# Kernel optimization log

Measured on AMD Instinct MI355X. Metric: run time of the kernel, lower is better.

The kernel has to match this reference:

```python
import jax, jax.numpy as jnp
import numpy as np

D_MODEL = 1024
NUM_HEADS = 16
D_K = D_MODEL // NUM_HEADS
D_FF = 4096
EPS = 1e-5


def _layer_norm(x, g, b):
    mu = jnp.mean(x, axis=-1, keepdims=True)
    var = jnp.mean(jnp.square(x - mu), axis=-1, keepdims=True)
    return (x - mu) * jax.lax.rsqrt(var + EPS) * g + b


def setup_inputs() -> dict:
    key = jax.random.key(0)
    ks = jax.random.split(key, 16)
    s = 0.02
    inp = {
        "x": jax.random.normal(ks[0], (2, 2048, D_MODEL), dtype=jnp.float32),
        # attention projections, torch Linear convention: W [out, in]
        "wq": jax.random.normal(ks[1], (D_MODEL, D_MODEL), dtype=jnp.float32) * s,
        "bq": jnp.zeros((D_MODEL,), jnp.float32),
        "wk": jax.random.normal(ks[2], (D_MODEL, D_MODEL), dtype=jnp.float32) * s,
        "bk": jnp.zeros((D_MODEL,), jnp.float32),
        "wv": jax.random.normal(ks[3], (D_MODEL, D_MODEL), dtype=jnp.float32) * s,
        "bv": jnp.zeros((D_MODEL,), jnp.float32),
        "wo": jax.random.normal(ks[4], (D_MODEL, D_MODEL), dtype=jnp.float32) * s,
        "bo": jnp.zeros((D_MODEL,), jnp.float32),
        "ln1_g": jnp.ones((D_MODEL,), jnp.float32),
        "ln1_b": jnp.zeros((D_MODEL,), jnp.float32),
        "w1": jax.random.normal(ks[5], (D_FF, D_MODEL), dtype=jnp.float32) * s,
        "b1": jnp.zeros((D_FF,), jnp.float32),
        "w2": jax.random.normal(ks[6], (D_MODEL, D_FF), dtype=jnp.float32) * s,
        "b2": jnp.zeros((D_MODEL,), jnp.float32),
        "ln2_g": jnp.ones((D_MODEL,), jnp.float32),
        "ln2_b": jnp.zeros((D_MODEL,), jnp.float32),
    }
    return inp


def reference(x, wq, bq, wk, bk, wv, bv, wo, bo, ln1_g, ln1_b,
              w1, b1, w2, b2, ln2_g, ln2_b):
    B, S, D = x.shape
    H, Dk = NUM_HEADS, D_K
    # projections -> [B, H, S, Dk]
    q = (x @ wq.T + bq).reshape(B, S, H, Dk).transpose(0, 2, 1, 3)
    k = (x @ wk.T + bk).reshape(B, S, H, Dk).transpose(0, 2, 1, 3)
    v = (x @ wv.T + bv).reshape(B, S, H, Dk).transpose(0, 2, 1, 3)
    # explicit [B,H,S,S] scores (faithful to source, memory-bound)
    scores = jnp.einsum("bhqd,bhkd->bhqk", q, k) / jnp.sqrt(jnp.float32(Dk))
    attn = jax.nn.softmax(scores, axis=-1)
    ctx = jnp.einsum("bhqk,bhkd->bhqd", attn, v)
    ctx = ctx.transpose(0, 2, 1, 3).reshape(B, S, D)
    attn_out = _layer_norm(ctx @ wo.T + bo + x, ln1_g, ln1_b)
    # feed-forward (post-LN residual), GELU (erf, torch default)
    h = jax.nn.gelu(attn_out @ w1.T + b1, approximate=False)
    ff = h @ w2.T + b2
    return _layer_norm(ff + attn_out, ln2_g, ln2_b)
```

## Files before the change

kernel.cpp:

```cpp
#include <hip/hip_runtime.h>
#include <math.h>

#define DM   1024
#define SL   2048
#define NB   2
#define NH   16
#define DKH  64
#define DFF  4096
#define NTOK 4096

typedef unsigned short u16;
typedef unsigned int u32;
typedef __attribute__((ext_vector_type(8))) short bf16x8;
typedef __attribute__((ext_vector_type(4))) float f32x4;
typedef __attribute__((ext_vector_type(16))) float f32x16;

typedef __attribute__((address_space(1))) void gvoid;
typedef __attribute__((address_space(3))) void lvoid;

#define QSCALE 0.18033688011112042f

__device__ __forceinline__ u16 f2bf(float f) {
  union { float f; unsigned u; } v; v.f = f;
  unsigned r = (v.u + 0x7fffu + ((v.u >> 16) & 1u)) >> 16;
  return (u16)r;
}
__device__ __forceinline__ float bf2f(u16 h) {
  union { unsigned u; float f; } v; v.u = ((unsigned)h) << 16; return v.f;
}
__device__ __forceinline__ void gld16(const u16* g, u16* l) {
  __builtin_amdgcn_global_load_lds((gvoid*)g, (lvoid*)l, 16, 0, 0);
}
__device__ __forceinline__ float gelu_fast(float v) {
  const float u = 2.302208f * (v + 0.044715f * v * v * v);
  const float e = __builtin_amdgcn_exp2f(u);
  return v - v * __builtin_amdgcn_rcpf(e + 1.0f);
}

__global__ __launch_bounds__(256)
void cvt_all(const float* __restrict__ x,  const float* __restrict__ wq,
             const float* __restrict__ wk, const float* __restrict__ wv,
             const float* __restrict__ wo, const float* __restrict__ w1,
             const float* __restrict__ w2,
             u16* __restrict__ xb, u16* __restrict__ wqb, u16* __restrict__ wkb,
             u16* __restrict__ wvb, u16* __restrict__ wob, u16* __restrict__ w1b,
             u16* __restrict__ w2b) {
  const int total = 4194304;
  for (int i = blockIdx.x * blockDim.x + threadIdx.x; i < total;
       i += gridDim.x * blockDim.x) {
    const float* src; u16* dst; int off;
    if      (i < 1048576) { src = x;  dst = xb;  off = i; }
    else if (i < 1310720) { src = wq; dst = wqb; off = i - 1048576; }
    else if (i < 1572864) { src = wk; dst = wkb; off = i - 1310720; }
    else if (i < 1835008) { src = wv; dst = wvb; off = i - 1572864; }
    else if (i < 2097152) { src = wo; dst = wob; off = i - 1835008; }
    else if (i < 3145728) { src = w1; dst = w1b; off = i - 2097152; }
    else                  { src = w2; dst = w2b; off = i - 3145728; }
    float4 v = ((const float4*)src)[off];
    ushort4 o = { f2bf(v.x), f2bf(v.y), f2bf(v.z), f2bf(v.w) };
    ((ushort4*)dst)[off] = o;
  }
}

#define BM 128
#define BN 128
#define BK 64

template <int EPI>
__global__ __launch_bounds__(256, 2)
void gemm_bt(const u16* __restrict__ A, const u16* __restrict__ W,
             const float* __restrict__ bias, const u16* __restrict__ residb,
             void* __restrict__ out, int M, int N, int K) {
  __shared__ u16 smem[2][2][BM * BK];
  const int tid = threadIdx.x;
  const int lane = tid & 63;
  const int wid  = tid >> 6;
  const int r16  = lane & 15;
  const int hi   = lane >> 4;
  const int wm = wid >> 1, wn = wid & 1;
  const int bm = blockIdx.x * BM;
  const int bn = blockIdx.y * BN;

  const int srow  = tid >> 3;
  const int sslot = (tid & 7) ^ (srow & 7);
  const size_t aoff = (size_t)(bm + srow) * K + sslot * 8;
  const size_t boff = (size_t)(bn + srow) * K + sslot * 8;

  f32x4 acc[4][4] = {};
  const int nk = K / BK;
  int cur = 0;

  auto STAGE = [&](int buf, int kt) {
    const u16* ga = A + aoff + kt * BK;
    const u16* gb = W + boff + kt * BK;
    u16* la = &smem[buf][0][wid * 512];
    u16* lb = &smem[buf][1][wid * 512];
#pragma unroll
    for (int i = 0; i < 4; ++i) {
      gld16(ga + (size_t)i * 32 * K, la + i * 2048);
      gld16(gb + (size_t)i * 32 * K, lb + i * 2048);
    }
  };

  STAGE(0, 0);
  __syncthreads();

  for (int kt = 0; kt < nk; ++kt) {
    if (kt + 1 < nk) STAGE(cur ^ 1, kt + 1);
    const u16* la = &smem[cur][0][0];
    const u16* lb = &smem[cur][1][0];
#pragma unroll
    for (int kk = 0; kk < 2; ++kk) {
      const int swz = ((kk * 4 + hi) ^ (r16 & 7)) * 8;
      bf16x8 af[4], bfr[4];
#pragma unroll
      for (int i = 0; i < 4; ++i)
        af[i] = *(const bf16x8*)&la[(wm * 64 + i * 16 + r16) * 64 + swz];
#pragma unroll
      for (int j = 0; j < 4; ++j)
        bfr[j] = *(const bf16x8*)&lb[(wn * 64 + j * 16 + r16) * 64 + swz];
      __builtin_amdgcn_s_setprio(1);
#pragma unroll
      for (int i = 0; i < 4; ++i)
#pragma unroll
        for (int j = 0; j < 4; ++j)
          acc[i][j] = __builtin_amdgcn_mfma_f32_16x16x32_bf16(af[i], bfr[j],
                                                              acc[i][j], 0, 0, 0);
      __builtin_amdgcn_s_setprio(0);
    }
    __syncthreads();
    cur ^= 1;
  }

#pragma unroll
  for (int i = 0; i < 4; ++i) {
#pragma unroll
    for (int j = 0; j < 4; ++j) {
      const int c  = bn + wn * 64 + j * 16 + r16;
      const int r0 = bm + wm * 64 + i * 16 + hi * 4;
      const float bv = bias[c];
#pragma unroll
      for (int rr = 0; rr < 4; ++rr) {
        const int r = r0 + rr;
        float v = acc[i][j][rr] + bv;
        if (EPI == 3) {
          ((u16*)out)[(size_t)r * N + c] =
              f2bf(v + bf2f(residb[(size_t)r * N + c]));
        } else {
          ((u16*)out)[(size_t)r * N + c] = f2bf(gelu_fast(v));
        }
      }
    }
  }
}

__global__ __launch_bounds__(256, 2)
void gemm_qkv(const u16* __restrict__ A, const u16* __restrict__ wq,
              const u16* __restrict__ wk, const u16* __restrict__ wv,
              const float* __restrict__ bq, const float* __restrict__ bk,
              const float* __restrict__ bv,
              u16* __restrict__ qo, u16* __restrict__ ko, u16* __restrict__ vo) {
  __shared__ u16 smem[2][2][BM * BK];
  const int tid = threadIdx.x;
  const int lane = tid & 63;
  const int wid  = tid >> 6;
  const int r16  = lane & 15;
  const int hi   = lane >> 4;
  const int wm = wid >> 1, wn = wid & 1;
  const int bm = blockIdx.x * BM;
  const int sel = blockIdx.y >> 3;
  const int bn  = (blockIdx.y & 7) * BN;
  const u16* W = sel == 0 ? wq : sel == 1 ? wk : wv;
  const float* bias = sel == 0 ? bq : sel == 1 ? bk : bv;
  const int K = DM, N = DM;

  const int srow  = tid >> 3;
  const int sslot = (tid & 7) ^ (srow & 7);
  const size_t aoff = (size_t)(bm + srow) * K + sslot * 8;
  const size_t boff = (size_t)(bn + srow) * K + sslot * 8;

  f32x4 acc[4][4] = {};
  int cur = 0;

  auto STAGE = [&](int buf, int kt) {
    const u16* ga = A + aoff + kt * BK;
    const u16* gb = W + boff + kt * BK;
    u16* la = &smem[buf][0][wid * 512];
    u16* lb = &smem[buf][1][wid * 512];
#pragma unroll
    for (int i = 0; i < 4; ++i) {
      gld16(ga + (size_t)i * 32 * K, la + i * 2048);
      gld16(gb + (size_t)i * 32 * K, lb + i * 2048);
    }
  };

  STAGE(0, 0);
  __syncthreads();

  for (int kt = 0; kt < 16; ++kt) {
    if (kt + 1 < 16) STAGE(cur ^ 1, kt + 1);
    const u16* la = &smem[cur][0][0];
    const u16* lb = &smem[cur][1][0];
#pragma unroll
    for (int kk = 0; kk < 2; ++kk) {
      const int swz = ((kk * 4 + hi) ^ (r16 & 7)) * 8;
      bf16x8 af[4], bfr[4];
#pragma unroll
      for (int i = 0; i < 4; ++i)
        af[i] = *(const bf16x8*)&la[(wm * 64 + i * 16 + r16) * 64 + swz];
#pragma unroll
      for (int j = 0; j < 4; ++j)
        bfr[j] = *(const bf16x8*)&lb[(wn * 64 + j * 16 + r16) * 64 + swz];
      __builtin_amdgcn_s_setprio(1);
#pragma unroll
      for (int i = 0; i < 4; ++i)
#pragma unroll
        for (int j = 0; j < 4; ++j)
          acc[i][j] = __builtin_amdgcn_mfma_f32_16x16x32_bf16(af[i], bfr[j],
                                                              acc[i][j], 0, 0, 0);
      __builtin_amdgcn_s_setprio(0);
    }
    __syncthreads();
    cur ^= 1;
  }

#pragma unroll
  for (int i = 0; i < 4; ++i) {
#pragma unroll
    for (int j = 0; j < 4; ++j) {
      const int c  = bn + wn * 64 + j * 16 + r16;
      const int r0 = bm + wm * 64 + i * 16 + hi * 4;
      const float bvv = bias[c];
#pragma unroll
      for (int rr = 0; rr < 4; ++rr) {
        const int r = r0 + rr;
        const float v = acc[i][j][rr] + bvv;
        if (sel == 0) {
          qo[(size_t)r * N + c] = f2bf(v * QSCALE);
        } else if (sel == 1) {
          ko[(size_t)r * N + c] = f2bf(v);
        } else {
          const int b = r >> 11, s = r & 2047;
          const int hh = c >> 6, dk = c & 63;
          vo[((size_t)((b * NH + hh) * DKH + dk)) * SL + s] = f2bf(v);
        }
      }
    }
  }
}

__global__ __launch_bounds__(256, 2)
void attn(const u16* __restrict__ q, const u16* __restrict__ k,
          const u16* __restrict__ vt, u16* __restrict__ ctx) {
  __shared__ u16 kl[2][64 * 64];
  __shared__ u16 vl[2][64 * 64];

  const int tid = threadIdx.x;
  const int lane = tid & 63, wid = tid >> 6;
  const int l31 = lane & 31, h = lane >> 5;
  const int rs = l31 & 7;
  const int bh = blockIdx.x, b = bh >> 4, hh = bh & 15;
  const int qg = blockIdx.y * 128 + wid * 32 + l31;

  bf16x8 qf[4];
#pragma unroll
  for (int kq = 0; kq < 4; ++kq)
    qf[kq] = *(const bf16x8*)(q + (size_t)(b * SL + qg) * DM + hh * DKH +
                              kq * 16 + h * 8);

  f32x16 o0 = {}, o1 = {};
  float mrun = -1e30f, lrun = 0.f;

  const int srow  = tid >> 3;
  const int sslot = (tid & 7) ^ (srow & 7);

  auto STAGE = [&](int buf, int t) {
    const u16* gk = k + (size_t)(b * SL + t * 64 + srow) * DM + hh * DKH + sslot * 8;
    const u16* gv = vt + (size_t)(bh * DKH + srow) * SL + t * 64 + sslot * 8;
    u16* lk = &kl[buf][wid * 512];
    u16* lv = &vl[buf][wid * 512];
#pragma unroll
    for (int i = 0; i < 2; ++i) {
      gld16(gk + (size_t)i * 32 * DM, lk + i * 2048);
      gld16(gv + (size_t)i * 32 * SL, lv + i * 2048);
    }
  };

  auto TILE = [&](int buf) {
    const u16* lk = kl[buf];
    const u16* lv = vl[buf];
    f32x16 s0 = {}, s1 = {};
    __builtin_amdgcn_s_setprio(1);
#pragma unroll
    for (int kq = 0; kq < 4; ++kq) {
      const int ls = 2 * kq + h;
      bf16x8 k0 = *(const bf16x8*)&lk[l31 * 64 + ((ls ^ rs) * 8)];
      bf16x8 k1 = *(const bf16x8*)&lk[(l31 + 32) * 64 + ((ls ^ rs) * 8)];
      s0 = __builtin_amdgcn_mfma_f32_32x32x16_bf16(k0, qf[kq], s0, 0, 0, 0);
      s1 = __builtin_amdgcn_mfma_f32_32x32x16_bf16(k1, qf[kq], s1, 0, 0, 0);
    }
    __builtin_amdgcn_s_setprio(0);

    float mx = fmaxf(s0[0], s0[1]);
#pragma unroll
    for (int r = 2; r < 16; ++r) mx = fmaxf(mx, s0[r]);
#pragma unroll
    for (int r = 0; r < 16; ++r) mx = fmaxf(mx, s1[r]);
    {
      float ta = mx, tb = mx;
      asm volatile("v_permlane32_swap_b32 %0, %1" : "+v"(ta), "+v"(tb));
      mx = fmaxf(ta, tb);
    }
    if (!__all(mx <= mrun + 11.0f)) {
      const float mn = fmaxf(mrun, mx);
      const float al = __builtin_amdgcn_exp2f(mrun - mn);
      mrun = mn;
      lrun *= al;
      o0 *= al; o1 *= al;
    }
    float lsum = 0.f;
#pragma unroll
    for (int r = 0; r < 16; ++r) {
      s0[r] = __builtin_amdgcn_exp2f(s0[r] - mrun); lsum += s0[r];
    }
#pragma unroll
    for (int r = 0; r < 16; ++r) {
      s1[r] = __builtin_amdgcn_exp2f(s1[r] - mrun); lsum += s1[r];
    }
    lrun += lsum;

    u32 A[16];
#pragma unroll
    for (int r = 0; r < 8; ++r)
      asm("v_cvt_pk_bf16_f32 %0, %1, %2"
          : "=v"(A[r]) : "v"(s0[2 * r]), "v"(s0[2 * r + 1]));
#pragma unroll
    for (int r = 0; r < 8; ++r)
      asm("v_cvt_pk_bf16_f32 %0, %1, %2"
          : "=v"(A[8 + r]) : "v"(s1[2 * r]), "v"(s1[2 * r + 1]));
#pragma unroll
    for (int g = 0; g < 4; ++g) {
      asm volatile("v_permlane32_swap_b32 %0, %1" : "+v"(A[4 * g + 0]), "+v"(A[4 * g + 2]));
      asm volatile("v_permlane32_swap_b32 %0, %1" : "+v"(A[4 * g + 1]), "+v"(A[4 * g + 3]));
    }

    __builtin_amdgcn_s_setprio(1);
#pragma unroll
    for (int ks = 0; ks < 4; ++ks) {
      union { u32 u[4]; bf16x8 hv; } pb;
      pb.u[0] = A[4 * ks + 0]; pb.u[1] = A[4 * ks + 1];
      pb.u[2] = A[4 * ks + 2]; pb.u[3] = A[4 * ks + 3];
      const int ls = 2 * ks + h;
      bf16x8 v0 = *(const bf16x8*)&lv[l31 * 64 + ((ls ^ rs) * 8)];
      bf16x8 v1 = *(const bf16x8*)&lv[(l31 + 32) * 64 + ((ls ^ rs) * 8)];
      o0 = __builtin_amdgcn_mfma_f32_32x32x16_bf16(v0, pb.hv, o0, 0, 0, 0);
      o1 = __builtin_amdgcn_mfma_f32_32x32x16_bf16(v1, pb.hv, o1, 0, 0, 0);
    }
    __builtin_amdgcn_s_setprio(0);
  };

  STAGE(0, 0);
  __syncthreads();
  int cur = 0;
  for (int t = 0; t < SL / 64; ++t) {
    if (t + 1 < SL / 64) STAGE(cur ^ 1, t + 1);
    TILE(cur);
    __syncthreads();
    cur ^= 1;
  }

  float ta = lrun, tb = lrun;
  asm volatile("v_permlane32_swap_b32 %0, %1" : "+v"(ta), "+v"(tb));
  const float rl = 1.f / (ta + tb);
  const size_t obase = (size_t)(b * SL + qg) * DM + hh * DKH;
#pragma unroll
  for (int df = 0; df < 2; ++df) {
#pragma unroll
    for (int r2 = 0; r2 < 4; ++r2) {
      const int dk0 = 8 * r2 + 4 * h + 32 * df;
      ushort4 st;
      if (df == 0) {
        st.x = f2bf(o0[4 * r2 + 0] * rl); st.y = f2bf(o0[4 * r2 + 1] * rl);
        st.z = f2bf(o0[4 * r2 + 2] * rl); st.w = f2bf(o0[4 * r2 + 3] * rl);
      } else {
        st.x = f2bf(o1[4 * r2 + 0] * rl); st.y = f2bf(o1[4 * r2 + 1] * rl);
        st.z = f2bf(o1[4 * r2 + 2] * rl); st.w = f2bf(o1[4 * r2 + 3] * rl);
      }
      *(ushort4*)(ctx + obase + dk0) = st;
    }
  }
}

template <int INBF>
__global__ __launch_bounds__(256)
void ln_k(const void* __restrict__ inp, const float* __restrict__ g,
          const float* __restrict__ be, float* __restrict__ outf,
          u16* __restrict__ outb) {
  const int row = blockIdx.x;
  const int tid = threadIdx.x;
  float4 x4;
  if (INBF) {
    ushort4 h4 = ((const ushort4*)((const u16*)inp + (size_t)row * DM))[tid];
    x4.x = bf2f(h4.x); x4.y = bf2f(h4.y); x4.z = bf2f(h4.z); x4.w = bf2f(h4.w);
  } else {
    x4 = ((const float4*)((const float*)inp + (size_t)row * DM))[tid];
  }
  float s  = x4.x + x4.y + x4.z + x4.w;
  float s2 = x4.x * x4.x + x4.y * x4.y + x4.z * x4.z + x4.w * x4.w;
#pragma unroll
  for (int d = 1; d < 64; d <<= 1) {
    s  += __shfl_xor(s, d);
    s2 += __shfl_xor(s2, d);
  }
  __shared__ float ps[8];
  const int wid = tid >> 6, lane = tid & 63;
  if (lane == 0) { ps[wid] = s; ps[wid + 4] = s2; }
  __syncthreads();
  const float S  = ps[0] + ps[1] + ps[2] + ps[3];
  const float S2 = ps[4] + ps[5] + ps[6] + ps[7];
  const float mu = S * (1.f / DM);
  const float var = S2 * (1.f / DM) - mu * mu;
  const float rstd = 1.f / sqrtf(var + 1e-5f);
  const float4 gv = ((const float4*)g)[tid];
  const float4 bv = ((const float4*)be)[tid];
  float4 o;
  o.x = (x4.x - mu) * rstd * gv.x + bv.x;
  o.y = (x4.y - mu) * rstd * gv.y + bv.y;
  o.z = (x4.z - mu) * rstd * gv.z + bv.z;
  o.w = (x4.w - mu) * rstd * gv.w + bv.w;
  if (outf) ((float4*)(outf + (size_t)row * DM))[tid] = o;
  if (outb) {
    ushort4 ob = { f2bf(o.x), f2bf(o.y), f2bf(o.z), f2bf(o.w) };
    ((ushort4*)(outb + (size_t)row * DM))[tid] = ob;
  }
}

extern "C" void kernel_launch(void* const* d_in, const int* in_sizes, int n_in,
                              void* d_out, int out_size, void* d_ws, size_t ws_size,
                              hipStream_t stream) {
  const float* x   = (const float*)d_in[0];
  const float* wq  = (const float*)d_in[1];
  const float* bq  = (const float*)d_in[2];
  const float* wk  = (const float*)d_in[3];
  const float* bk  = (const float*)d_in[4];
  const float* wv  = (const float*)d_in[5];
  const float* bv  = (const float*)d_in[6];
  const float* wo  = (const float*)d_in[7];
  const float* bo  = (const float*)d_in[8];
  const float* g1  = (const float*)d_in[9];
  const float* be1 = (const float*)d_in[10];
  const float* w1  = (const float*)d_in[11];
  const float* b1  = (const float*)d_in[12];
  const float* w2  = (const float*)d_in[13];
  const float* b2  = (const float*)d_in[14];
  const float* g2  = (const float*)d_in[15];
  const float* be2 = (const float*)d_in[16];

  if (ws_size < ((size_t)80 << 20)) return;

  char* ws = (char*)d_ws;
  u16*  xb   = (u16*)(ws);
  u16*  wqb  = (u16*)(ws + ((size_t)8  << 20));
  u16*  wkb  = (u16*)(ws + ((size_t)10 << 20));
  u16*  wvb  = (u16*)(ws + ((size_t)12 << 20));
  u16*  wob  = (u16*)(ws + ((size_t)14 << 20));
  u16*  w1b  = (u16*)(ws + ((size_t)16 << 20));
  u16*  w2b  = (u16*)(ws + ((size_t)24 << 20));
  u16*  qbuf = (u16*)(ws + ((size_t)32 << 20));
  u16*  kbuf = (u16*)(ws + ((size_t)40 << 20));
  u16*  vtb  = (u16*)(ws + ((size_t)48 << 20));
  u16*  ctx  = (u16*)(ws + ((size_t)56 << 20));
  u16*  oresb = (u16*)(ws + ((size_t)64 << 20));
  u16*  ffb   = (u16*)(ws + ((size_t)72 << 20));
  u16*  aob  = xb;
  u16*  hb   = qbuf;

  float* out = (float*)d_out;
  dim3 blk(256);

  cvt_all<<<2048, blk, 0, stream>>>(x, wq, wk, wv, wo, w1, w2,
                                    xb, wqb, wkb, wvb, wob, w1b, w2b);
  gemm_qkv<<<dim3(32, 24), blk, 0, stream>>>(xb, wqb, wkb, wvb, bq, bk, bv,
                                             qbuf, kbuf, vtb);
  attn<<<dim3(32, 16), blk, 0, stream>>>(qbuf, kbuf, vtb, ctx);
  gemm_bt<3><<<dim3(32, 8), blk, 0, stream>>>(ctx, wob, bo, xb, oresb,
                                              NTOK, DM, DM);
  ln_k<1><<<4096, blk, 0, stream>>>(oresb, g1, be1, nullptr, aob);
  gemm_bt<4><<<dim3(32, 32), blk, 0, stream>>>(aob, w1b, b1, nullptr,
                                               hb, NTOK, DFF, DM);
  gemm_bt<3><<<dim3(32, 8), blk, 0, stream>>>(hb, w2b, b2, aob, ffb,
                                              NTOK, DM, DFF);
  ln_k<1><<<4096, blk, 0, stream>>>(ffb, g2, be2, out, nullptr);
}
```

Before: 226.1 us.

## Process 128-key tiles per attention iteration with tree-reduced max and sum

The flash-attention loop now stages and processes two 64-key sub-tiles (128 keys) per iteration, which halves the number of barriers and online-softmax rescale checks. Row max and exp-sum use tree reductions with v_max3 instead of serial chains. LDS use doubles to 64KB per block, and register pressure rises with four score accumulators, which may hurt occupancy at the 2-blocks-per-CU launch bound.

Result: no change. 228.7 us (+1.1%).

```diff
diff --git a/kernel.cpp b/kernel.cpp
--- a/kernel.cpp
+++ b/kernel.cpp
@@ -35,6 +35,28 @@
   const float u = 2.302208f * (v + 0.044715f * v * v * v);
   const float e = __builtin_amdgcn_exp2f(u);
   return v - v * __builtin_amdgcn_rcpf(e + 1.0f);
+}
+__device__ __forceinline__ float max3f(float a, float b, float c) {
+  float d;
+  asm("v_max3_f32 %0, %1, %2, %3" : "=v"(d) : "v"(a), "v"(b), "v"(c));
+  return d;
+}
+__device__ __forceinline__ float rmax16(const f32x16& v) {
+  const float a0 = max3f(v[0], v[1], v[2]);
+  const float a1 = max3f(v[3], v[4], v[5]);
+  const float a2 = max3f(v[6], v[7], v[8]);
+  const float a3 = max3f(v[9], v[10], v[11]);
+  const float a4 = max3f(v[12], v[13], v[14]);
+  const float b0 = max3f(a0, a1, a2);
+  const float b1 = max3f(a3, a4, v[15]);
+  return fmaxf(b0, b1);
+}
+__device__ __forceinline__ float rsum16(const f32x16& v) {
+  const float s0 = (v[0] + v[1]) + (v[2] + v[3]);
+  const float s1 = (v[4] + v[5]) + (v[6] + v[7]);
+  const float s2 = (v[8] + v[9]) + (v[10] + v[11]);
+  const float s3 = (v[12] + v[13]) + (v[14] + v[15]);
+  return (s0 + s1) + (s2 + s3);
 }
 
 __global__ __launch_bounds__(256)
@@ -252,8 +274,8 @@
 __global__ __launch_bounds__(256, 2)
 void attn(const u16* __restrict__ q, const u16* __restrict__ k,
           const u16* __restrict__ vt, u16* __restrict__ ctx) {
-  __shared__ u16 kl[2][64 * 64];
-  __shared__ u16 vl[2][64 * 64];
+  __shared__ u16 kl[2][2][64 * 64];
+  __shared__ u16 vl[2][2][64 * 64];
 
   const int tid = threadIdx.x;
   const int lane = tid & 63, wid = tid >> 6;
@@ -274,38 +296,43 @@
   const int srow  = tid >> 3;
   const int sslot = (tid & 7) ^ (srow & 7);
 
-  auto STAGE = [&](int buf, int t) {
-    const u16* gk = k + (size_t)(b * SL + t * 64 + srow) * DM + hh * DKH + sslot * 8;
-    const u16* gv = vt + (size_t)(bh * DKH + srow) * SL + t * 64 + sslot * 8;
-    u16* lk = &kl[buf][wid * 512];
-    u16* lv = &vl[buf][wid * 512];
-#pragma unroll
-    for (int i = 0; i < 2; ++i) {
-      gld16(gk + (size_t)i * 32 * DM, lk + i * 2048);
-      gld16(gv + (size_t)i * 32 * SL, lv + i * 2048);
+  auto STAGE = [&](int buf, int u) {
+#pragma unroll
+    for (int sub = 0; sub < 2; ++sub) {
+      const int kv0 = u * 128 + sub * 64;
+      const u16* gk = k + (size_t)(b * SL + kv0 + srow) * DM + hh * DKH + sslot * 8;
+      const u16* gv = vt + (size_t)(bh * DKH + srow) * SL + kv0 + sslot * 8;
+      u16* lk = &kl[buf][sub][wid * 512];
+      u16* lv = &vl[buf][sub][wid * 512];
+#pragma unroll
+      for (int i = 0; i < 2; ++i) {
+        gld16(gk + (size_t)i * 32 * DM, lk + i * 2048);
+        gld16(gv + (size_t)i * 32 * SL, lv + i * 2048);
+      }
     }
   };
 
-  auto TILE = [&](int buf) {
-    const u16* lk = kl[buf];
-    const u16* lv = vl[buf];
-    f32x16 s0 = {}, s1 = {};
+  auto TILE2 = [&](int buf) {
+    f32x16 sA0 = {}, sA1 = {}, sB0 = {}, sB1 = {};
     __builtin_amdgcn_s_setprio(1);
 #pragma unroll
     for (int kq = 0; kq < 4; ++kq) {
       const int ls = 2 * kq + h;
-      bf16x8 k0 = *(const bf16x8*)&lk[l31 * 64 + ((ls ^ rs) * 8)];
-      bf16x8 k1 = *(const bf16x8*)&lk[(l31 + 32) * 64 + ((ls ^ rs) * 8)];
-      s0 = __builtin_amdgcn_mfma_f32_32x32x16_bf16(k0, qf[kq], s0, 0, 0, 0);
-      s1 = __builtin_amdgcn_mfma_f32_32x32x16_bf16(k1, qf[kq], s1, 0, 0, 0);
+      const u16* lkA = kl[buf][0];
+      const u16* lkB = kl[buf][1];
+      bf16x8 a0 = *(const bf16x8*)&lkA[l31 * 64 + ((ls ^ rs) * 8)];
+      bf16x8 a1 = *(const bf16x8*)&lkA[(l31 + 32) * 64 + ((ls ^ rs) * 8)];
+      bf16x8 b0 = *(const bf16x8*)&lkB[l31 * 64 + ((ls ^ rs) * 8)];
+      bf16x8 b1 = *(const bf16x8*)&lkB[(l31 + 32) * 64 + ((ls ^ rs) * 8)];
+      sA0 = __builtin_amdgcn_mfma_f32_32x32x16_bf16(a0, qf[kq], sA0, 0, 0, 0);
+      sA1 = __builtin_amdgcn_mfma_f32_32x32x16_bf16(a1, qf[kq], sA1, 0, 0, 0);
+      sB0 = __builtin_amdgcn_mfma_f32_32x32x16_bf16(b0, qf[kq], sB0, 0, 0, 0);
+      sB1 = __builtin_amdgcn_mfma_f32_32x32x16_bf16(b1, qf[kq], sB1, 0, 0, 0);
     }
     __builtin_amdgcn_s_setprio(0);
 
-    float mx = fmaxf(s0[0], s0[1]);
-#pragma unroll
-    for (int r = 2; r < 16; ++r) mx = fmaxf(mx, s0[r]);
-#pragma unroll
-    for (int r = 0; r < 16; ++r) mx = fmaxf(mx, s1[r]);
+    float mx = fmaxf(fmaxf(rmax16(sA0), rmax16(sA1)),
+                     fmaxf(rmax16(sB0), rmax16(sB1)));
     {
       float ta = mx, tb = mx;
       asm volatile("v_permlane32_swap_b32 %0, %1" : "+v"(ta), "+v"(tb));
@@ -318,43 +345,51 @@
       lrun *= al;
       o0 *= al; o1 *= al;
     }
-    float lsum = 0.f;
 #pragma unroll
     for (int r = 0; r < 16; ++r) {
-      s0[r] = __builtin_amdgcn_exp2f(s0[r] - mrun); lsum += s0[r];
-    }
-#pragma unroll
-    for (int r = 0; r < 16; ++r) {
-      s1[r] = __builtin_amdgcn_exp2f(s1[r] - mrun); lsum += s1[r];
-    }
-    lrun += lsum;
-
-    u32 A[16];
-#pragma unroll
-    for (int r = 0; r < 8; ++r)
+      sA0[r] = __builtin_amdgcn_exp2f(sA0[r] - mrun);
+      sA1[r] = __builtin_amdgcn_exp2f(sA1[r] - mrun);
+      sB0[r] = __builtin_amdgcn_exp2f(sB0[r] - mrun);
+      sB1[r] = __builtin_amdgcn_exp2f(sB1[r] - mrun);
+    }
+    lrun += (rsum16(sA0) + rsum16(sA1)) + (rsum16(sB0) + rsum16(sB1));
+
+    u32 A0[16], A1[16];
+#pragma unroll
+    for (int r = 0; r < 8; ++r) {
       asm("v_cvt_pk_bf16_f32 %0, %1, %2"
-          : "=v"(A[r]) : "v"(s0[2 * r]), "v"(s0[2 * r + 1]));
-#pragma unroll
-    for (int r = 0; r < 8; ++r)
+          : "=v"(A0[r]) : "v"(sA0[2 * r]), "v"(sA0[2 * r + 1]));
       asm("v_cvt_pk_bf16_f32 %0, %1, %2"
-          : "=v"(A[8 + r]) : "v"(s1[2 * r]), "v"(s1[2 * r + 1]));
+          : "=v"(A0[8 + r]) : "v"(sA1[2 * r]), "v"(sA1[2 * r + 1]));
+      asm("v_cvt_pk_bf16_f32 %0, %1, %2"
+          : "=v"(A1[r]) : "v"(sB0[2 * r]), "v"(sB0[2 * r + 1]));
+      asm("v_cvt_pk_bf16_f32 %0, %1, %2"
+          : "=v"(A1[8 + r]) : "v"(sB1[2 * r]), "v"(sB1[2 * r + 1]));
+    }
 #pragma unroll
     for (int g = 0; g < 4; ++g) {
-      asm volatile("v_permlane32_swap_b32 %0, %1" : "+v"(A[4 * g + 0]), "+v"(A[4 * g + 2]));
-      asm volatile("v_permlane32_swap_b32 %0, %1" : "+v"(A[4 * g + 1]), "+v"(A[4 * g + 3]));
+      asm volatile("v_permlane32_swap_b32 %0, %1" : "+v"(A0[4 * g + 0]), "+v"(A0[4 * g + 2]));
+      asm volatile("v_permlane32_swap_b32 %0, %1" : "+v"(A0[4 * g + 1]), "+v"(A0[4 * g + 3]));
+      asm volatile("v_permlane32_swap_b32 %0, %1" : "+v"(A1[4 * g + 0]), "+v"(A1[4 * g + 2]));
+      asm volatile("v_permlane32_swap_b32 %0, %1" : "+v"(A1[4 * g + 1]), "+v"(A1[4 * g + 3]));
     }
 
     __builtin_amdgcn_s_setprio(1);
 #pragma unroll
-    for (int ks = 0; ks < 4; ++ks) {
-      union { u32 u[4]; bf16x8 hv; } pb;
-      pb.u[0] = A[4 * ks + 0]; pb.u[1] = A[4 * ks + 1];
-      pb.u[2] = A[4 * ks + 2]; pb.u[3] = A[4 * ks + 3];
-      const int ls = 2 * ks + h;
-      bf16x8 v0 = *(const bf16x8*)&lv[l31 * 64 + ((ls ^ rs) * 8)];
-      bf16x8 v1 = *(const bf16x8*)&lv[(l31 + 32) * 64 + ((ls ^ rs) * 8)];
-      o0 = __builtin_amdgcn_mfma_f32_32x32x16_bf16(v0, pb.hv, o0, 0, 0, 0);
-      o1 = __builtin_amdgcn_mfma_f32_32x32x16_bf16(v1, pb.hv, o1, 0, 0, 0);
+    for (int sub = 0; sub < 2; ++sub) {
+      const u16* lv = vl[buf][sub];
+      const u32* Ax = sub ? A1 : A0;
+#pragma unroll
+      for (int ks = 0; ks < 4; ++ks) {
+        union { u32 u[4]; bf16x8 hv; } pb;
+        pb.u[0] = Ax[4 * ks + 0]; pb.u[1] = Ax[4 * ks + 1];
+        pb.u[2] = Ax[4 * ks + 2]; pb.u[3] = Ax[4 * ks + 3];
+        const int ls = 2 * ks + h;
+        bf16x8 v0 = *(const bf16x8*)&lv[l31 * 64 + ((ls ^ rs) * 8)];
+        bf16x8 v1 = *(const bf16x8*)&lv[(l31 + 32) * 64 + ((ls ^ rs) * 8)];
+        o0 = __builtin_amdgcn_mfma_f32_32x32x16_bf16(v0, pb.hv, o0, 0, 0, 0);
+        o1 = __builtin_amdgcn_mfma_f32_32x32x16_bf16(v1, pb.hv, o1, 0, 0, 0);
+      }
     }
     __builtin_amdgcn_s_setprio(0);
   };
@@ -362,9 +397,9 @@
   STAGE(0, 0);
   __syncthreads();
   int cur = 0;
-  for (int t = 0; t < SL / 64; ++t) {
-    if (t + 1 < SL / 64) STAGE(cur ^ 1, t + 1);
-    TILE(cur);
+  for (int u = 0; u < SL / 128; ++u) {
+    if (u + 1 < SL / 128) STAGE(cur ^ 1, u + 1);
+    TILE2(cur);
     __syncthreads();
     cur ^= 1;
   }
```

## Load attention K/V fragments directly from global memory, dropping LDS staging

Applied to the files above, without the earlier changes.

The attention kernel no longer stages K and V tiles into double-buffered shared memory with global_load_lds and block barriers. Each wave now reads its K and V MFMA fragments straight from global memory into registers, and occupancy is raised to 3 blocks per CU. The row max and row sum are also rewritten as v_max3 and tree reductions. The aim is to remove barrier and LDS overhead, but every wave now fetches K/V separately with no overlap from prefetch, so it leans on L2 bandwidth and latency hiding from the extra waves.

Result: slower. 299.0 us (+32.2%).

```diff
diff --git a/kernel.cpp b/kernel.cpp
--- a/kernel.cpp
+++ b/kernel.cpp
@@ -35,6 +35,28 @@
   const float u = 2.302208f * (v + 0.044715f * v * v * v);
   const float e = __builtin_amdgcn_exp2f(u);
   return v - v * __builtin_amdgcn_rcpf(e + 1.0f);
+}
+__device__ __forceinline__ float max3f(float a, float b, float c) {
+  float d;
+  asm("v_max3_f32 %0, %1, %2, %3" : "=v"(d) : "v"(a), "v"(b), "v"(c));
+  return d;
+}
+__device__ __forceinline__ float rmax16(const f32x16& v) {
+  const float a0 = max3f(v[0], v[1], v[2]);
+  const float a1 = max3f(v[3], v[4], v[5]);
+  const float a2 = max3f(v[6], v[7], v[8]);
+  const float a3 = max3f(v[9], v[10], v[11]);
+  const float a4 = max3f(v[12], v[13], v[14]);
+  const float b0 = max3f(a0, a1, a2);
+  const float b1 = max3f(a3, a4, v[15]);
+  return fmaxf(b0, b1);
+}
+__device__ __forceinline__ float rsum16(const f32x16& v) {
+  const float s0 = (v[0] + v[1]) + (v[2] + v[3]);
+  const float s1 = (v[4] + v[5]) + (v[6] + v[7]);
+  const float s2 = (v[8] + v[9]) + (v[10] + v[11]);
+  const float s3 = (v[12] + v[13]) + (v[14] + v[15]);
+  return (s0 + s1) + (s2 + s3);
 }
 
 __global__ __launch_bounds__(256)
@@ -249,16 +271,12 @@
   }
 }
 
-__global__ __launch_bounds__(256, 2)
+__global__ __launch_bounds__(256, 3)
 void attn(const u16* __restrict__ q, const u16* __restrict__ k,
           const u16* __restrict__ vt, u16* __restrict__ ctx) {
-  __shared__ u16 kl[2][64 * 64];
-  __shared__ u16 vl[2][64 * 64];
-
   const int tid = threadIdx.x;
   const int lane = tid & 63, wid = tid >> 6;
   const int l31 = lane & 31, h = lane >> 5;
-  const int rs = l31 & 7;
   const int bh = blockIdx.x, b = bh >> 4, hh = bh & 15;
   const int qg = blockIdx.y * 128 + wid * 32 + l31;
 
@@ -271,41 +289,35 @@
   f32x16 o0 = {}, o1 = {};
   float mrun = -1e30f, lrun = 0.f;
 
-  const int srow  = tid >> 3;
-  const int sslot = (tid & 7) ^ (srow & 7);
-
-  auto STAGE = [&](int buf, int t) {
-    const u16* gk = k + (size_t)(b * SL + t * 64 + srow) * DM + hh * DKH + sslot * 8;
-    const u16* gv = vt + (size_t)(bh * DKH + srow) * SL + t * 64 + sslot * 8;
-    u16* lk = &kl[buf][wid * 512];
-    u16* lv = &vl[buf][wid * 512];
-#pragma unroll
-    for (int i = 0; i < 2; ++i) {
-      gld16(gk + (size_t)i * 32 * DM, lk + i * 2048);
-      gld16(gv + (size_t)i * 32 * SL, lv + i * 2048);
-    }
-  };
-
-  auto TILE = [&](int buf) {
-    const u16* lk = kl[buf];
-    const u16* lv = vl[buf];
+  const u16* kbase = k + (size_t)b * SL * DM + (size_t)hh * DKH;
+  const u16* vbase = vt + (size_t)bh * DKH * SL;
+
+  for (int t = 0; t < SL / 64; ++t) {
+    const u16* kt_ = kbase + (size_t)(t * 64 + l31) * DM + h * 8;
+    bf16x8 kf0[4], kf1[4];
+#pragma unroll
+    for (int kq = 0; kq < 4; ++kq) {
+      kf0[kq] = *(const bf16x8*)(kt_ + kq * 16);
+      kf1[kq] = *(const bf16x8*)(kt_ + (size_t)32 * DM + kq * 16);
+    }
     f32x16 s0 = {}, s1 = {};
     __builtin_amdgcn_s_setprio(1);
 #pragma unroll
     for (int kq = 0; kq < 4; ++kq) {
-      const int ls = 2 * kq + h;
-      bf16x8 k0 = *(const bf16x8*)&lk[l31 * 64 + ((ls ^ rs) * 8)];
-      bf16x8 k1 = *(const bf16x8*)&lk[(l31 + 32) * 64 + ((ls ^ rs) * 8)];
-      s0 = __builtin_amdgcn_mfma_f32_32x32x16_bf16(k0, qf[kq], s0, 0, 0, 0);
-      s1 = __builtin_amdgcn_mfma_f32_32x32x16_bf16(k1, qf[kq], s1, 0, 0, 0);
+      s0 = __builtin_amdgcn_mfma_f32_32x32x16_bf16(kf0[kq], qf[kq], s0, 0, 0, 0);
+      s1 = __builtin_amdgcn_mfma_f32_32x32x16_bf16(kf1[kq], qf[kq], s1, 0, 0, 0);
     }
     __builtin_amdgcn_s_setprio(0);
 
-    float mx = fmaxf(s0[0], s0[1]);
-#pragma unroll
-    for (int r = 2; r < 16; ++r) mx = fmaxf(mx, s0[r]);
-#pragma unroll
-    for (int r = 0; r < 16; ++r) mx = fmaxf(mx, s1[r]);
+    const u16* vt_ = vbase + (size_t)l31 * SL + t * 64 + h * 8;
+    bf16x8 vf0[4], vf1[4];
+#pragma unroll
+    for (int ks = 0; ks < 4; ++ks) {
+      vf0[ks] = *(const bf16x8*)(vt_ + ks * 16);
+      vf1[ks] = *(const bf16x8*)(vt_ + (size_t)32 * SL + ks * 16);
+    }
+
+    float mx = fmaxf(rmax16(s0), rmax16(s1));
     {
       float ta = mx, tb = mx;
       asm volatile("v_permlane32_swap_b32 %0, %1" : "+v"(ta), "+v"(tb));
@@ -318,26 +330,21 @@
       lrun *= al;
       o0 *= al; o1 *= al;
     }
-    float lsum = 0.f;
 #pragma unroll
     for (int r = 0; r < 16; ++r) {
-      s0[r] = __builtin_amdgcn_exp2f(s0[r] - mrun); lsum += s0[r];
-    }
-#pragma unroll
-    for (int r = 0; r < 16; ++r) {
-      s1[r] = __builtin_amdgcn_exp2f(s1[r] - mrun); lsum += s1[r];
-    }
-    lrun += lsum;
+      s0[r] = __builtin_amdgcn_exp2f(s0[r] - mrun);
+      s1[r] = __builtin_amdgcn_exp2f(s1[r] - mrun);
+    }
+    lrun += rsum16(s0) + rsum16(s1);
 
     u32 A[16];
 #pragma unroll
-    for (int r = 0; r < 8; ++r)
+    for (int r = 0; r < 8; ++r) {
       asm("v_cvt_pk_bf16_f32 %0, %1, %2"
           : "=v"(A[r]) : "v"(s0[2 * r]), "v"(s0[2 * r + 1]));
-#pragma unroll
-    for (int r = 0; r < 8; ++r)
       asm("v_cvt_pk_bf16_f32 %0, %1, %2"
           : "=v"(A[8 + r]) : "v"(s1[2 * r]), "v"(s1[2 * r + 1]));
+    }
 #pragma unroll
     for (int g = 0; g < 4; ++g) {
       asm volatile("v_permlane32_swap_b32 %0, %1" : "+v"(A[4 * g + 0]), "+v"(A[4 * g + 2]));
@@ -350,23 +357,10 @@
       union { u32 u[4]; bf16x8 hv; } pb;
       pb.u[0] = A[4 * ks + 0]; pb.u[1] = A[4 * ks + 1];
       pb.u[2] = A[4 * ks + 2]; pb.u[3] = A[4 * ks + 3];
-      const int ls = 2 * ks + h;
-      bf16x8 v0 = *(const bf16x8*)&lv[l31 * 64 + ((ls ^ rs) * 8)];
-      bf16x8 v1 = *(const bf16x8*)&lv[(l31 + 32) * 64 + ((ls ^ rs) * 8)];
-      o0 = __builtin_amdgcn_mfma_f32_32x32x16_bf16(v0, pb.hv, o0, 0, 0, 0);
-      o1 = __builtin_amdgcn_mfma_f32_32x32x16_bf16(v1, pb.hv, o1, 0, 0, 0);
+      o0 = __builtin_amdgcn_mfma_f32_32x32x16_bf16(vf0[ks], pb.hv, o0, 0, 0, 0);
+      o1 = __builtin_amdgcn_mfma_f32_32x32x16_bf16(vf1[ks], pb.hv, o1, 0, 0, 0);
     }
     __builtin_amdgcn_s_setprio(0);
-  };
-
-  STAGE(0, 0);
-  __syncthreads();
-  int cur = 0;
-  for (int t = 0; t < SL / 64; ++t) {
-    if (t + 1 < SL / 64) STAGE(cur ^ 1, t + 1);
-    TILE(cur);
-    __syncthreads();
-    cur ^= 1;
   }
 
   float ta = lrun, tb = lrun;
```
